# Kernel tuning notes

Hardware: AMD Instinct MI355X
Metric: run time of the kernel (lower is better)

The kernel has to match this reference:

```python
import jax, jax.numpy as jnp
import numpy as np

VOCAB = 50257
F = 1024
RANK = 8


def setup_inputs() -> dict:
    key = jax.random.key(0)
    k_idx, k_emb, k_a = jax.random.split(key, 3)
    index_tensor = jax.random.randint(k_idx, (8, 4096), 0, VOCAB, dtype=jnp.int64)
    emb_weight = jax.random.normal(k_emb, (VOCAB, F), dtype=jnp.float32)
    # kaiming_uniform_ with nonlinearity='linear': bound = sqrt(3)*sqrt(1/fan_in), fan_in=RANK
    bound = float(np.sqrt(3.0) * np.sqrt(1.0 / RANK))
    A = jax.random.uniform(k_a, (F, RANK), minval=-bound, maxval=bound, dtype=jnp.float32)
    B = jnp.zeros((RANK, F), dtype=jnp.float32)
    bias = jnp.zeros((F,), dtype=jnp.float32)
    return {"index_tensor": index_tensor, "emb_weight": emb_weight, "A": A, "B": B, "bias": bias}


def reference(index_tensor, emb_weight, A, B, bias):
    # base = E[idx]; out = base @ (I + A@B) + bias == base + (base@A)@B + bias
    base = emb_weight[index_tensor]                      # [b, s, F] gather
    low = jnp.einsum('bsf,fr->bsr', base, A)             # [b, s, R]
    return base + jnp.einsum('bsr,rf->bsf', low, B) + bias
```

## Files before the change

kernel.cpp:

```cpp
#include <hip/hip_runtime.h>


constexpr int F  = 1024;
constexpr int R  = 8;
constexpr int F4 = F / 4;
constexpr int TPB  = 256;
constexpr int NBLK = 2048;

__global__ __launch_bounds__(TPB, 4)
void lora_emb_kernel(const int* __restrict__ idx,
                     const float* __restrict__ emb,
                     const float* __restrict__ A,
                     const float* __restrict__ Bm,
                     const float* __restrict__ bias,
                     float* __restrict__ out,
                     int ntok)
{
    __shared__ float ldsP[2][4][R];

    const int lane    = threadIdx.x & 63;
    const int quarter = threadIdx.x >> 6;
    const int f4      = quarter * 64 + lane;

    float a_frag[4][8];
    #pragma unroll
    for (int j = 0; j < 4; ++j) {
        const float* ap = A + (size_t)(4 * f4 + j) * R;
        const float4 lo = *reinterpret_cast<const float4*>(ap);
        const float4 hi = *reinterpret_cast<const float4*>(ap + 4);
        a_frag[j][0] = lo.x; a_frag[j][1] = lo.y; a_frag[j][2] = lo.z; a_frag[j][3] = lo.w;
        a_frag[j][4] = hi.x; a_frag[j][5] = hi.y; a_frag[j][6] = hi.z; a_frag[j][7] = hi.w;
    }
    float b_frag[8][4];
    #pragma unroll
    for (int r = 0; r < 8; ++r) {
        const float4 b = *reinterpret_cast<const float4*>(Bm + (size_t)r * F + 4 * f4);
        b_frag[r][0] = b.x; b_frag[r][1] = b.y; b_frag[r][2] = b.z; b_frag[r][3] = b.w;
    }
    const float4 bi = *reinterpret_cast<const float4*>(bias + 4 * f4);

    const float4* emb4 = reinterpret_cast<const float4*>(emb);
    float4*       out4 = reinterpret_cast<float4*>(out);

    const int stride = gridDim.x;
    int t = blockIdx.x;
    if (t >= ntok) return;

    int   t1      = t + stride;
    int   row_nxt = (t1 < ntok) ? idx[t1] : 0;
    float4 v      = emb4[(size_t)idx[t] * F4 + f4];

    const bool s1 = (lane & 1) != 0;
    const bool s2 = (lane & 2) != 0;
    const bool s4 = (lane & 4) != 0;
    const int  rr = ((lane & 1) << 2) | (lane & 2) | ((lane >> 2) & 1);

    int buf = 0;
    while (true) {
        const bool hasn = (t1 < ntok);
        float4 vn;
        if (hasn) vn = emb4[(size_t)row_nxt * F4 + f4];
        const int t2     = t1 + stride;
        const int row_n2 = (t2 < ntok) ? idx[t2] : 0;

        float p[8];
        #pragma unroll
        for (int r = 0; r < 8; ++r)
            p[r] = v.x * a_frag[0][r] + v.y * a_frag[1][r]
                 + v.z * a_frag[2][r] + v.w * a_frag[3][r];

        float q[4];
        #pragma unroll
        for (int j = 0; j < 4; ++j) {
            const float send = s1 ? p[j]     : p[j + 4];
            const float keep = s1 ? p[j + 4] : p[j];
            q[j] = keep + __shfl_xor(send, 1, 64);
        }
        float w2[2];
        #pragma unroll
        for (int j = 0; j < 2; ++j) {
            const float send = s2 ? q[j]     : q[j + 2];
            const float keep = s2 ? q[j + 2] : q[j];
            w2[j] = keep + __shfl_xor(send, 2, 64);
        }
        float s = (s4 ? w2[1] : w2[0]) + __shfl_xor(s4 ? w2[0] : w2[1], 4, 64);
        s += __shfl_xor(s, 8, 64);
        s += __shfl_xor(s, 16, 64);
        s += __shfl_xor(s, 32, 64);

        if (lane < 8) ldsP[buf][quarter][rr] = s;
        __syncthreads();

        float pall[8];
        {
            const float4* pb = reinterpret_cast<const float4*>(&ldsP[buf][0][0]);
            const float4 l0 = pb[0], h0 = pb[1];
            const float4 l1 = pb[2], h1 = pb[3];
            const float4 l2 = pb[4], h2 = pb[5];
            const float4 l3 = pb[6], h3 = pb[7];
            pall[0] = l0.x + l1.x + l2.x + l3.x;
            pall[1] = l0.y + l1.y + l2.y + l3.y;
            pall[2] = l0.z + l1.z + l2.z + l3.z;
            pall[3] = l0.w + l1.w + l2.w + l3.w;
            pall[4] = h0.x + h1.x + h2.x + h3.x;
            pall[5] = h0.y + h1.y + h2.y + h3.y;
            pall[6] = h0.z + h1.z + h2.z + h3.z;
            pall[7] = h0.w + h1.w + h2.w + h3.w;
        }

        const float vv[4] = { v.x, v.y, v.z, v.w };
        const float bb[4] = { bi.x, bi.y, bi.z, bi.w };
        float o[4];
        #pragma unroll
        for (int c = 0; c < 4; ++c) {
            float acc = vv[c] + bb[c];
            #pragma unroll
            for (int r = 0; r < 8; ++r) acc += pall[r] * b_frag[r][c];
            o[c] = acc;
        }
        out4[(size_t)t * F4 + f4] = make_float4(o[0], o[1], o[2], o[3]);

        if (!hasn) break;
        v = vn; t = t1; t1 = t2; row_nxt = row_n2; buf ^= 1;
    }
}

extern "C" void kernel_launch(void* const* d_in, const int* in_sizes, int n_in,
                              void* d_out, int out_size, void* d_ws, size_t ws_size,
                              hipStream_t stream) {
    const int*   idx  = (const int*)  d_in[0];
    const float* emb  = (const float*)d_in[1];
    const float* A    = (const float*)d_in[2];
    const float* Bm   = (const float*)d_in[3];
    const float* bias = (const float*)d_in[4];
    float* out = (float*)d_out;

    const int ntok = in_sizes[0];
    int blocks = NBLK;
    if (blocks > ntok) blocks = ntok;

    hipLaunchKernelGGL(lora_emb_kernel, dim3(blocks), dim3(TPB), 0, stream,
                       idx, emb, A, Bm, bias, out, ntok);
}
```

Before: 323.0 us.

## Deepen gather prefetch to two tokens, use raw barrier and nontemporal stores

Extends the software pipeline so each block keeps two embedding rows in flight ahead of the current token instead of one, hiding more of the random gather latency. Replaces __syncthreads with an explicit lgkmcnt wait plus s_barrier, so outstanding global loads are not drained at the barrier. Output writes use nontemporal stores to avoid polluting cache. This costs extra registers, which may lower occupancy.

New measurement: 318.6 us. Within noise of the previous version (-1.4%).

```diff
diff --git a/kernel.cpp b/kernel.cpp
--- a/kernel.cpp
+++ b/kernel.cpp
@@ -1,5 +1,7 @@
 #include <hip/hip_runtime.h>
 
+
+typedef float f32x4 __attribute__((ext_vector_type(4)));
 
 constexpr int F  = 1024;
 constexpr int R  = 8;
@@ -26,29 +28,34 @@
     #pragma unroll
     for (int j = 0; j < 4; ++j) {
         const float* ap = A + (size_t)(4 * f4 + j) * R;
-        const float4 lo = *reinterpret_cast<const float4*>(ap);
-        const float4 hi = *reinterpret_cast<const float4*>(ap + 4);
+        const f32x4 lo = *reinterpret_cast<const f32x4*>(ap);
+        const f32x4 hi = *reinterpret_cast<const f32x4*>(ap + 4);
         a_frag[j][0] = lo.x; a_frag[j][1] = lo.y; a_frag[j][2] = lo.z; a_frag[j][3] = lo.w;
         a_frag[j][4] = hi.x; a_frag[j][5] = hi.y; a_frag[j][6] = hi.z; a_frag[j][7] = hi.w;
     }
     float b_frag[8][4];
     #pragma unroll
     for (int r = 0; r < 8; ++r) {
-        const float4 b = *reinterpret_cast<const float4*>(Bm + (size_t)r * F + 4 * f4);
+        const f32x4 b = *reinterpret_cast<const f32x4*>(Bm + (size_t)r * F + 4 * f4);
         b_frag[r][0] = b.x; b_frag[r][1] = b.y; b_frag[r][2] = b.z; b_frag[r][3] = b.w;
     }
-    const float4 bi = *reinterpret_cast<const float4*>(bias + 4 * f4);
+    const f32x4 bi = *reinterpret_cast<const f32x4*>(bias + 4 * f4);
 
-    const float4* emb4 = reinterpret_cast<const float4*>(emb);
-    float4*       out4 = reinterpret_cast<float4*>(out);
+    const f32x4* emb4 = reinterpret_cast<const f32x4*>(emb);
+    f32x4*       out4 = reinterpret_cast<f32x4*>(out);
 
     const int stride = gridDim.x;
-    int t = blockIdx.x;
-    if (t >= ntok) return;
+    int t0 = blockIdx.x;
+    if (t0 >= ntok) return;
 
-    int   t1      = t + stride;
-    int   row_nxt = (t1 < ntok) ? idx[t1] : 0;
-    float4 v      = emb4[(size_t)idx[t] * F4 + f4];
+    int t1 = t0 + stride;
+    int t2 = t1 + stride;
+    f32x4 v = emb4[(size_t)idx[t0] * F4 + f4];
+    f32x4 vn;
+    const bool h1_init = (t1 < ntok);
+    if (h1_init) vn = emb4[(size_t)idx[t1] * F4 + f4];
+    int row2 = (t2 < ntok) ? idx[t2] : 0;
+    bool h1 = h1_init;
 
     const bool s1 = (lane & 1) != 0;
     const bool s2 = (lane & 2) != 0;
@@ -57,11 +64,11 @@
 
     int buf = 0;
     while (true) {
-        const bool hasn = (t1 < ntok);
-        float4 vn;
-        if (hasn) vn = emb4[(size_t)row_nxt * F4 + f4];
-        const int t2     = t1 + stride;
-        const int row_n2 = (t2 < ntok) ? idx[t2] : 0;
+        const bool h2 = (t2 < ntok);
+        f32x4 vn2;
+        if (h2) vn2 = emb4[(size_t)row2 * F4 + f4];
+        const int t3   = t2 + stride;
+        const int row3 = (t3 < ntok) ? idx[t3] : 0;
 
         float p[8];
         #pragma unroll
@@ -89,23 +96,25 @@
         s += __shfl_xor(s, 32, 64);
 
         if (lane < 8) ldsP[buf][quarter][rr] = s;
-        __syncthreads();
+        asm volatile("s_waitcnt lgkmcnt(0)" ::: "memory");
+        __builtin_amdgcn_s_barrier();
+        asm volatile("" ::: "memory");
 
         float pall[8];
         {
-            const float4* pb = reinterpret_cast<const float4*>(&ldsP[buf][0][0]);
-            const float4 l0 = pb[0], h0 = pb[1];
-            const float4 l1 = pb[2], h1 = pb[3];
-            const float4 l2 = pb[4], h2 = pb[5];
-            const float4 l3 = pb[6], h3 = pb[7];
+            const f32x4* pb = reinterpret_cast<const f32x4*>(&ldsP[buf][0][0]);
+            const f32x4 l0 = pb[0], h0 = pb[1];
+            const f32x4 l1 = pb[2], h1r = pb[3];
+            const f32x4 l2 = pb[4], h2r = pb[5];
+            const f32x4 l3 = pb[6], h3r = pb[7];
             pall[0] = l0.x + l1.x + l2.x + l3.x;
             pall[1] = l0.y + l1.y + l2.y + l3.y;
             pall[2] = l0.z + l1.z + l2.z + l3.z;
             pall[3] = l0.w + l1.w + l2.w + l3.w;
-            pall[4] = h0.x + h1.x + h2.x + h3.x;
-            pall[5] = h0.y + h1.y + h2.y + h3.y;
-            pall[6] = h0.z + h1.z + h2.z + h3.z;
-            pall[7] = h0.w + h1.w + h2.w + h3.w;
+            pall[4] = h0.x + h1r.x + h2r.x + h3r.x;
+            pall[5] = h0.y + h1r.y + h2r.y + h3r.y;
+            pall[6] = h0.z + h1r.z + h2r.z + h3r.z;
+            pall[7] = h0.w + h1r.w + h2r.w + h3r.w;
         }
 
         const float vv[4] = { v.x, v.y, v.z, v.w };
@@ -118,10 +127,13 @@
             for (int r = 0; r < 8; ++r) acc += pall[r] * b_frag[r][c];
             o[c] = acc;
         }
-        out4[(size_t)t * F4 + f4] = make_float4(o[0], o[1], o[2], o[3]);
+        f32x4 ov; ov.x = o[0]; ov.y = o[1]; ov.z = o[2]; ov.w = o[3];
+        __builtin_nontemporal_store(ov, out4 + (size_t)t0 * F4 + f4);
 
-        if (!hasn) break;
-        v = vn; t = t1; t1 = t2; row_nxt = row_n2; buf ^= 1;
+        if (!h1) break;
+        v = vn; vn = vn2; h1 = h2;
+        t0 = t1; t1 = t2; t2 = t3; row2 = row3;
+        buf ^= 1;
     }
 }
 
```
